# Kernel optimization log

Measured on AMD Instinct MI355X. Metric: run time of the kernel, lower is better.

The kernel has to match this reference:

```python
import jax, jax.numpy as jnp
import numpy as np

DIM = 1024
N_HEADS = 16
HEAD_DIM = DIM // N_HEADS
MLP = 4 * DIM
B, N = 2, 2048
LN_EPS = 1e-5


def setup_inputs() -> dict:
    key = jax.random.key(0)
    ks = jax.random.split(key, 12)
    s = lambda fan_in: 1.0 / np.sqrt(fan_in)
    return {
        "x": jax.random.normal(ks[0], (B, N, DIM), dtype=jnp.float32),
        "qkv_w": jax.random.uniform(ks[1], (3 * DIM, DIM), jnp.float32, -s(DIM), s(DIM)),
        "out_w": jax.random.uniform(ks[2], (DIM, DIM), jnp.float32, -s(DIM), s(DIM)),
        "out_b": jax.random.uniform(ks[3], (DIM,), jnp.float32, -s(DIM), s(DIM)),
        "ff_w1": jax.random.uniform(ks[4], (MLP, DIM), jnp.float32, -s(DIM), s(DIM)),
        "ff_b1": jax.random.uniform(ks[5], (MLP,), jnp.float32, -s(DIM), s(DIM)),
        "ff_w2": jax.random.uniform(ks[6], (DIM, MLP), jnp.float32, -s(MLP), s(MLP)),
        "ff_b2": jax.random.uniform(ks[7], (DIM,), jnp.float32, -s(MLP), s(MLP)),
        "ln1_w": jnp.ones((DIM,), jnp.float32),
        "ln1_b": jnp.zeros((DIM,), jnp.float32),
        "ln2_w": jnp.ones((DIM,), jnp.float32),
        "ln2_b": jnp.zeros((DIM,), jnp.float32),
    }


def _layernorm(x, w, b):
    mu = jnp.mean(x, axis=-1, keepdims=True)
    var = jnp.mean(jnp.square(x - mu), axis=-1, keepdims=True)
    return (x - mu) * jax.lax.rsqrt(var + LN_EPS) * w + b


def reference(x, qkv_w, out_w, out_b, ff_w1, ff_b1, ff_w2, ff_b2,
              ln1_w, ln1_b, ln2_w, ln2_b):
    Bx, Nx, D = x.shape
    scale = HEAD_DIM ** -0.5
    x_ln = _layernorm(x, ln1_w, ln1_b)
    qkv = (x_ln @ qkv_w.T).reshape(Bx, Nx, 3, N_HEADS, HEAD_DIM)
    qkv = jnp.transpose(qkv, (2, 0, 3, 1, 4))  # [3, B, H, N, hd]
    q, k, v = qkv[0], qkv[1], qkv[2]
    attn = jnp.einsum('bhid,bhjd->bhij', q, k) * scale
    attn = jax.nn.softmax(attn, axis=-1)
    o = jnp.einsum('bhij,bhjd->bhid', attn, v)
    o = jnp.transpose(o, (0, 2, 1, 3)).reshape(Bx, Nx, D)
    x = x + o @ out_w.T + out_b
    x_ln2 = _layernorm(x, ln2_w, ln2_b)
    h = jax.nn.silu(x_ln2 @ ff_w1.T + ff_b1)
    x = x + h @ ff_w2.T + ff_b2
    return x
```

## Files before the change

### kernel.cpp

```cpp
#include <hip/hip_runtime.h>
#include <stdint.h>

#define DIM   1024
#define NH    16
#define HD    64
#define SEQ   2048
#define BATCH 2
#define MROWS 4096
#define MLPD  4096
#define LN_EPS 1e-5f
#define QSCALE 0.18033688011112042f

typedef _Float16 f16;
typedef _Float16 half8 __attribute__((ext_vector_type(8)));
typedef _Float16 half4 __attribute__((ext_vector_type(4)));
typedef float f32x4 __attribute__((ext_vector_type(4)));

__device__ __forceinline__ void async_cp16(const void* g, void* l) {
  __builtin_amdgcn_global_load_lds(
      (const __attribute__((address_space(1))) unsigned int*)g,
      (__attribute__((address_space(3))) unsigned int*)l, 16, 0, 0);
}

__global__ __launch_bounds__(256) void cvt_all_kernel(
    const float* __restrict__ w0, const float* __restrict__ w1,
    const float* __restrict__ w2, const float* __restrict__ w3,
    f16* __restrict__ d0, f16* __restrict__ d1, f16* __restrict__ d2,
    f16* __restrict__ d3) {
  int blk = blockIdx.x;
  const float* s;
  f16* d;
  int base;
  if (blk < 3072)      { s = w0; d = d0; base = blk; }
  else if (blk < 4096) { s = w1; d = d1; base = blk - 3072; }
  else if (blk < 8192) { s = w2; d = d2; base = blk - 4096; }
  else                 { s = w3; d = d3; base = blk - 8192; }
  int i = (base * 256 + threadIdx.x) * 4;
  float4 v = *(const float4*)(s + i);
  half4 o = { (f16)v.x, (f16)v.y, (f16)v.z, (f16)v.w };
  *(half4*)(d + i) = o;
}

__global__ __launch_bounds__(256) void ln_kernel(const float* __restrict__ x,
    const float* __restrict__ w, const float* __restrict__ b, f16* __restrict__ out) {
  __shared__ float red[8];
  int row = blockIdx.x, t = threadIdx.x;
  const float4 v = ((const float4*)(x + (size_t)row * DIM))[t];
  float s1 = v.x + v.y + v.z + v.w;
  float s2 = v.x * v.x + v.y * v.y + v.z * v.z + v.w * v.w;
#pragma unroll
  for (int m = 32; m; m >>= 1) { s1 += __shfl_xor(s1, m); s2 += __shfl_xor(s2, m); }
  if ((t & 63) == 0) { red[t >> 6] = s1; red[4 + (t >> 6)] = s2; }
  __syncthreads();
  s1 = red[0] + red[1] + red[2] + red[3];
  s2 = red[4] + red[5] + red[6] + red[7];
  float mu = s1 * (1.f / DIM);
  float rs = rsqrtf(s2 * (1.f / DIM) - mu * mu + LN_EPS);
  float4 wv = ((const float4*)w)[t];
  float4 bv = ((const float4*)b)[t];
  half4 o = { (f16)((v.x - mu) * rs * wv.x + bv.x), (f16)((v.y - mu) * rs * wv.y + bv.y),
              (f16)((v.z - mu) * rs * wv.z + bv.z), (f16)((v.w - mu) * rs * wv.w + bv.w) };
  ((half4*)(out + (size_t)row * DIM))[t] = o;
}

template <int MODE, int TM, int TN, int BK, int GSWAP>
__global__ __launch_bounds__(256, (TN == 64) ? 4 : 1) void gemm_bt(
    const f16* __restrict__ A, const f16* __restrict__ W,
    const float* __restrict__ bias, const float* __restrict__ resid,
    float* __restrict__ outf, f16* __restrict__ outq, f16* __restrict__ outk,
    f16* __restrict__ outv, int K) {
  constexpr int IT = (TN == 128) ? (TM / 32) : (TM / 64);
  constexpr int MSUB = IT * 16;
  constexpr int CPR = BK / 8;
  constexpr int RPP = 256 / CPR;
  __shared__ __align__(16) f16 As[TM * BK];
  __shared__ __align__(16) f16 Bs[TN * BK];
  const int t = threadIdx.x;
  const int wave = t >> 6, lane = t & 63;
  const int n16 = lane & 15, quad = lane >> 4;
  const int tile_m = (GSWAP ? blockIdx.x : blockIdx.y) * TM;
  const int tile_n = (GSWAP ? blockIdx.y : blockIdx.x) * TN;
  const int wm = (TN == 128) ? (wave >> 1) : wave;
  const int wn = (TN == 128) ? (wave & 1) : 0;
  const int srow = lane / CPR, spos = lane & (CPR - 1);
  const f32x4 zero4 = {0.f, 0.f, 0.f, 0.f};

  f32x4 acc[IT][4];
#pragma unroll
  for (int i = 0; i < IT; i++)
#pragma unroll
    for (int j = 0; j < 4; j++) acc[i][j] = zero4;

  for (int k0 = 0; k0 < K; k0 += BK) {
#pragma unroll
    for (int q = 0; q < TM / RPP; q++) {
      int r = q * RPP + wave * (64 / CPR) + srow;
      int c = spos ^ (r & (CPR - 1));
      async_cp16(A + (size_t)(tile_m + r) * K + k0 + c * 8, &As[q * 2048 + wave * 512]);
    }
#pragma unroll
    for (int q = 0; q < TN / RPP; q++) {
      int r = q * RPP + wave * (64 / CPR) + srow;
      int c = spos ^ (r & (CPR - 1));
      async_cp16(W + (size_t)(tile_n + r) * K + k0 + c * 8, &Bs[q * 2048 + wave * 512]);
    }
    __syncthreads();
#pragma unroll
    for (int kk = 0; kk < BK / 32; kk++) {
      half8 af[IT], bfr[4];
#pragma unroll
      for (int i = 0; i < IT; i++) {
        int row = wm * MSUB + i * 16 + n16;
        int c = (kk * 4 + quad) ^ (row & (CPR - 1));
        af[i] = *(const half8*)&As[row * BK + c * 8];
      }
#pragma unroll
      for (int j = 0; j < 4; j++) {
        int row = wn * 64 + j * 16 + n16;
        int c = (kk * 4 + quad) ^ (row & (CPR - 1));
        bfr[j] = *(const half8*)&Bs[row * BK + c * 8];
      }
#pragma unroll
      for (int i = 0; i < IT; i++)
#pragma unroll
        for (int j = 0; j < 4; j++)
          acc[i][j] = __builtin_amdgcn_mfma_f32_16x16x32_f16(af[i], bfr[j], acc[i][j], 0, 0, 0);
    }
    __syncthreads();
  }

#pragma unroll
  for (int i = 0; i < IT; i++) {
#pragma unroll
    for (int j = 0; j < 4; j++) {
      int gcol = tile_n + wn * 64 + j * 16 + n16;
      int grow0 = tile_m + wm * MSUB + i * 16 + quad * 4;
      if constexpr (MODE == 0) {
        int tsel = gcol >> 10, h = (gcol >> 6) & 15, d = gcol & 63;
        int bb = grow0 >> 11, nn0 = grow0 & 2047;
        if (tsel == 2) {
          half4 o;
#pragma unroll
          for (int r = 0; r < 4; r++) o[r] = (f16)acc[i][j][r];
          *(half4*)&outv[(((size_t)bb * NH + h) * HD + d) * SEQ + nn0] = o;
        } else {
          f16* dst = (tsel == 0) ? outq : outk;
          float sc = (tsel == 0) ? QSCALE : 1.0f;
#pragma unroll
          for (int r = 0; r < 4; r++)
            dst[(((size_t)bb * NH + h) * SEQ + nn0 + r) * HD + d] = (f16)(acc[i][j][r] * sc);
        }
      } else if constexpr (MODE == 1) {
#pragma unroll
        for (int r = 0; r < 4; r++) {
          size_t idx = (size_t)(grow0 + r) * DIM + gcol;
          outf[idx] = acc[i][j][r] + bias[gcol] + resid[idx];
        }
      } else {
#pragma unroll
        for (int r = 0; r < 4; r++) {
          float z = acc[i][j][r] + bias[gcol];
          float sg = 1.f / (1.f + __expf(-z));
          outq[(size_t)(grow0 + r) * MLPD + gcol] = (f16)(z * sg);
        }
      }
    }
  }
}

__global__ __launch_bounds__(256, 4) void attn_kernel(const f16* __restrict__ qg,
    const f16* __restrict__ kg, const f16* __restrict__ vtg,
    float* __restrict__ op, float* __restrict__ lp) {
  __shared__ __align__(16) f16 Ks[64 * 64];
  __shared__ __align__(16) f16 Vs[64 * 64];
  const int bh = blockIdx.z, kc = blockIdx.y, q0 = blockIdx.x * 128;
  const int t = threadIdx.x, wave = t >> 6, lane = t & 63;
  const int n16 = lane & 15, quad = lane >> 4;
  const int srow = lane >> 3, spos = lane & 7;
  const f32x4 zero4 = {0.f, 0.f, 0.f, 0.f};

  half8 qf[2][2];
#pragma unroll
  for (int qt = 0; qt < 2; qt++) {
    const f16* qr = qg + ((size_t)bh * SEQ + q0 + wave * 32 + qt * 16 + n16) * HD + quad * 8;
    qf[qt][0] = *(const half8*)qr;
    qf[qt][1] = *(const half8*)(qr + 32);
  }

  f32x4 oc[2][4];
#pragma unroll
  for (int qt = 0; qt < 2; qt++)
#pragma unroll
    for (int dt = 0; dt < 4; dt++) oc[qt][dt] = zero4;
  float ls[2] = {0.f, 0.f};

  for (int kt64 = 0; kt64 < 16; kt64++) {
    const int kv0 = kc * 1024 + kt64 * 64;
#pragma unroll
    for (int p = 0; p < 2; p++) {
      int r = p * 32 + wave * 8 + srow;
      int c = spos ^ (r & 7);
      async_cp16(kg + ((size_t)bh * SEQ + kv0 + r) * HD + c * 8, &Ks[p * 2048 + wave * 512]);
      async_cp16(vtg + ((size_t)bh * HD + r) * SEQ + kv0 + c * 8, &Vs[p * 2048 + wave * 512]);
    }
    __syncthreads();

    f32x4 st[4][2];
#pragma unroll
    for (int kt = 0; kt < 4; kt++) {
      int row = kt * 16 + n16;
      half8 kf0 = *(const half8*)&Ks[row * 64 + (quad ^ (row & 7)) * 8];
      half8 kf1 = *(const half8*)&Ks[row * 64 + ((quad + 4) ^ (row & 7)) * 8];
#pragma unroll
      for (int qt = 0; qt < 2; qt++) {
        f32x4 z = zero4;
        z = __builtin_amdgcn_mfma_f32_16x16x32_f16(kf0, qf[qt][0], z, 0, 0, 0);
        z = __builtin_amdgcn_mfma_f32_16x16x32_f16(kf1, qf[qt][1], z, 0, 0, 0);
        st[kt][qt] = z;
      }
    }

    half4 pf[2][4];
#pragma unroll
    for (int qt = 0; qt < 2; qt++)
#pragma unroll
      for (int kt = 0; kt < 4; kt++) {
        half4 p4;
        float s0 = __builtin_exp2f(st[kt][qt][0]);
        float s1 = __builtin_exp2f(st[kt][qt][1]);
        float s2 = __builtin_exp2f(st[kt][qt][2]);
        float s3 = __builtin_exp2f(st[kt][qt][3]);
        p4[0] = (f16)s0; p4[1] = (f16)s1; p4[2] = (f16)s2; p4[3] = (f16)s3;
        ls[qt] += (s0 + s1) + (s2 + s3);
        pf[qt][kt] = p4;
      }

#pragma unroll
    for (int kt = 0; kt < 4; kt++) {
      half4 va[4];
#pragma unroll
      for (int dt = 0; dt < 4; dt++) {
        int row = dt * 16 + n16;
        int phys = (kt * 2 + (quad >> 1)) ^ (row & 7);
        va[dt] = *(const half4*)&Vs[row * 64 + phys * 8 + (quad & 1) * 4];
      }
#pragma unroll
      for (int dt = 0; dt < 4; dt++)
#pragma unroll
        for (int qt = 0; qt < 2; qt++)
          oc[qt][dt] = __builtin_amdgcn_mfma_f32_16x16x16f16(va[dt], pf[qt][kt], oc[qt][dt], 0, 0, 0);
    }
    __syncthreads();
  }

  const int b = bh >> 4, h = bh & 15;
#pragma unroll
  for (int qt = 0; qt < 2; qt++) {
    float l = ls[qt];
    l += __shfl_xor(l, 16);
    l += __shfl_xor(l, 32);
    int q = q0 + wave * 32 + qt * 16 + n16;
    int row = b * SEQ + q;
#pragma unroll
    for (int dt = 0; dt < 4; dt++)
      *(f32x4*)&op[((size_t)kc * MROWS + row) * DIM + h * HD + dt * 16 + quad * 4] = oc[qt][dt];
    if (quad == 0) lp[((size_t)kc * BATCH * NH + bh) * SEQ + q] = l;
  }
}

__global__ __launch_bounds__(256) void attn_reduce_kernel(const float* __restrict__ op,
    const float* __restrict__ lp, f16* __restrict__ obuf) {
  int row = blockIdx.x;
  int t = threadIdx.x;
  int b = row >> 11, q = row & 2047;
  int h = t >> 4;
  size_t base = (size_t)row * DIM + t * 4;
  float4 o1 = *(const float4*)&op[base];
  float4 o2 = *(const float4*)&op[(size_t)MROWS * DIM + base];
  size_t li = ((size_t)b * NH + h) * SEQ + q;
  float l = lp[li] + lp[(size_t)BATCH * NH * SEQ + li];
  float inv = 1.f / l;
  half4 o = { (f16)((o1.x + o2.x) * inv), (f16)((o1.y + o2.y) * inv),
              (f16)((o1.z + o2.z) * inv), (f16)((o1.w + o2.w) * inv) };
  *(half4*)&obuf[base] = o;
}

extern "C" void kernel_launch(void* const* d_in, const int* in_sizes, int n_in,
                              void* d_out, int out_size, void* d_ws, size_t ws_size,
                              hipStream_t stream) {
  const float* x     = (const float*)d_in[0];
  const float* qkv_w = (const float*)d_in[1];
  const float* out_w = (const float*)d_in[2];
  const float* out_b = (const float*)d_in[3];
  const float* ff_w1 = (const float*)d_in[4];
  const float* ff_b1 = (const float*)d_in[5];
  const float* ff_w2 = (const float*)d_in[6];
  const float* ff_b2 = (const float*)d_in[7];
  const float* ln1_w = (const float*)d_in[8];
  const float* ln1_b = (const float*)d_in[9];
  const float* ln2_w = (const float*)d_in[10];
  const float* ln2_b = (const float*)d_in[11];
  float* out = (float*)d_out;

  char* p = (char*)d_ws;
  size_t off = 0;
  auto alloc = [&](size_t bytes) {
    void* r = p + off;
    off += (bytes + 255) & ~(size_t)255;
    return r;
  };
  f16* wqkv = (f16*)alloc((size_t)3 * DIM * DIM * 2);
  f16* wout = (f16*)alloc((size_t)DIM * DIM * 2);
  f16* wf1  = (f16*)alloc((size_t)MLPD * DIM * 2);
  f16* wf2  = (f16*)alloc((size_t)MLPD * DIM * 2);
  f16* xln  = (f16*)alloc((size_t)MROWS * DIM * 2);
  f16* qb   = (f16*)alloc((size_t)MROWS * DIM * 2);
  f16* kb   = (f16*)alloc((size_t)MROWS * DIM * 2);
  f16* vtb  = (f16*)alloc((size_t)MROWS * DIM * 2);
  f16* obuf = (f16*)alloc((size_t)MROWS * DIM * 2);
  float* x1 = (float*)alloc((size_t)MROWS * DIM * 4);
  f16* hbuf = (f16*)alloc((size_t)MROWS * MLPD * 2);
  float* lp = (float*)alloc((size_t)2 * BATCH * NH * SEQ * 4);
  f16* x1ln = xln;
  float* opa = (float*)hbuf;

  cvt_all_kernel<<<12288, 256, 0, stream>>>(qkv_w, out_w, ff_w1, ff_w2,
                                            wqkv, wout, wf1, wf2);
  ln_kernel<<<MROWS, 256, 0, stream>>>(x, ln1_w, ln1_b, xln);
  gemm_bt<0, 128, 128, 64, 0><<<dim3(3 * DIM / 128, MROWS / 128), 256, 0, stream>>>(
      xln, wqkv, nullptr, nullptr, nullptr, qb, kb, vtb, DIM);
  attn_kernel<<<dim3(SEQ / 128, 2, BATCH * NH), 256, 0, stream>>>(qb, kb, vtb, opa, lp);
  attn_reduce_kernel<<<MROWS, 256, 0, stream>>>(opa, lp, obuf);
  gemm_bt<1, 128, 64, 128, 1><<<dim3(MROWS / 128, DIM / 64), 256, 0, stream>>>(
      obuf, wout, out_b, x, x1, nullptr, nullptr, nullptr, DIM);
  ln_kernel<<<MROWS, 256, 0, stream>>>(x1, ln2_w, ln2_b, x1ln);
  gemm_bt<2, 128, 128, 64, 0><<<dim3(MLPD / 128, MROWS / 128), 256, 0, stream>>>(
      x1ln, wf1, ff_b1, nullptr, nullptr, hbuf, nullptr, nullptr, DIM);
  gemm_bt<1, 128, 64, 128, 1><<<dim3(MROWS / 128, DIM / 64), 256, 0, stream>>>(
      hbuf, wf2, ff_b2, x1, out, nullptr, nullptr, nullptr, MLPD);
}
```

Measured before the change: 350.5 us.

## Use 16x16x32 MFMA for PV by permuting K rows and packing P conversions

In the attention kernel, the P·V product now uses 16x16x32 f16 MFMAs in place of pairs of 16x16x16 ones. K rows are permuted during the async load so the S accumulator layout lines up with the K=32 operand layout. V fragments are read as half8 instead of half4, and the exp results are packed to f16 with cvt_pkrtz. This halves the PV MFMA instruction count and the number of LDS reads. In exchange it switches to round-toward-zero f16 conversion and depends on a non-obvious row permutation being correct.

```diff
diff --git a/kernel.cpp b/kernel.cpp
--- a/kernel.cpp
+++ b/kernel.cpp
@@ -14,7 +14,12 @@
 typedef _Float16 f16;
 typedef _Float16 half8 __attribute__((ext_vector_type(8)));
 typedef _Float16 half4 __attribute__((ext_vector_type(4)));
+typedef _Float16 half2 __attribute__((ext_vector_type(2)));
 typedef float f32x4 __attribute__((ext_vector_type(4)));
+
+__device__ __forceinline__ half2 pk_f16(float a, float b) {
+  return __builtin_bit_cast(half2, __builtin_amdgcn_cvt_pkrtz(a, b));
+}
 
 __device__ __forceinline__ void async_cp16(const void* g, void* l) {
   __builtin_amdgcn_global_load_lds(
@@ -200,7 +205,8 @@
     for (int p = 0; p < 2; p++) {
       int r = p * 32 + wave * 8 + srow;
       int c = spos ^ (r & 7);
-      async_cp16(kg + ((size_t)bh * SEQ + kv0 + r) * HD + c * 8, &Ks[p * 2048 + wave * 512]);
+      int rk = (r & 0x23) | ((r & 0x0C) << 1) | ((r & 0x10) >> 2);
+      async_cp16(kg + ((size_t)bh * SEQ + kv0 + rk) * HD + c * 8, &Ks[p * 2048 + wave * 512]);
       async_cp16(vtg + ((size_t)bh * HD + r) * SEQ + kv0 + c * 8, &Vs[p * 2048 + wave * 512]);
     }
     __syncthreads();
@@ -220,35 +226,37 @@
       }
     }
 
-    half4 pf[2][4];
+    union { half8 v; half2 h[4]; } pf[2][2];
 #pragma unroll
     for (int qt = 0; qt < 2; qt++)
 #pragma unroll
-      for (int kt = 0; kt < 4; kt++) {
-        half4 p4;
-        float s0 = __builtin_exp2f(st[kt][qt][0]);
-        float s1 = __builtin_exp2f(st[kt][qt][1]);
-        float s2 = __builtin_exp2f(st[kt][qt][2]);
-        float s3 = __builtin_exp2f(st[kt][qt][3]);
-        p4[0] = (f16)s0; p4[1] = (f16)s1; p4[2] = (f16)s2; p4[3] = (f16)s3;
-        ls[qt] += (s0 + s1) + (s2 + s3);
-        pf[qt][kt] = p4;
-      }
-
-#pragma unroll
-    for (int kt = 0; kt < 4; kt++) {
-      half4 va[4];
+      for (int kt2 = 0; kt2 < 2; kt2++) {
+        f32x4 a = st[kt2 * 2][qt], b = st[kt2 * 2 + 1][qt];
+        float e0 = __builtin_exp2f(a[0]), e1 = __builtin_exp2f(a[1]);
+        float e2 = __builtin_exp2f(a[2]), e3 = __builtin_exp2f(a[3]);
+        float e4 = __builtin_exp2f(b[0]), e5 = __builtin_exp2f(b[1]);
+        float e6 = __builtin_exp2f(b[2]), e7 = __builtin_exp2f(b[3]);
+        ls[qt] += ((e0 + e1) + (e2 + e3)) + ((e4 + e5) + (e6 + e7));
+        pf[qt][kt2].h[0] = pk_f16(e0, e1);
+        pf[qt][kt2].h[1] = pk_f16(e2, e3);
+        pf[qt][kt2].h[2] = pk_f16(e4, e5);
+        pf[qt][kt2].h[3] = pk_f16(e6, e7);
+      }
+
+#pragma unroll
+    for (int kt2 = 0; kt2 < 2; kt2++) {
+      half8 va[4];
 #pragma unroll
       for (int dt = 0; dt < 4; dt++) {
         int row = dt * 16 + n16;
-        int phys = (kt * 2 + (quad >> 1)) ^ (row & 7);
-        va[dt] = *(const half4*)&Vs[row * 64 + phys * 8 + (quad & 1) * 4];
+        int phys = (kt2 * 4 + quad) ^ (row & 7);
+        va[dt] = *(const half8*)&Vs[row * 64 + phys * 8];
       }
 #pragma unroll
       for (int dt = 0; dt < 4; dt++)
 #pragma unroll
         for (int qt = 0; qt < 2; qt++)
-          oc[qt][dt] = __builtin_amdgcn_mfma_f32_16x16x16f16(va[dt], pf[qt][kt], oc[qt][dt], 0, 0, 0);
+          oc[qt][dt] = __builtin_amdgcn_mfma_f32_16x16x32_f16(va[dt], pf[qt][kt2].v, oc[qt][dt], 0, 0, 0);
     }
     __syncthreads();
   }
```

Result: no change. 354.4 us (+1.1%).
